# Performance work log

Measured on AMD Instinct MI355X. Metric: run time of the kernel, lower is better.

The kernel has to match this reference:

```python
import jax, jax.numpy as jnp
import numpy as np

E = 8        # n_experts
TOP_K = 2    # n_activated_experts
B, T, C = 4, 2048, 2048   # batch, seq, d_model
F = 5632     # expert FFN hidden (SwiGLU)


def setup_inputs() -> dict:
    key = jax.random.key(0)
    k = jax.random.split(key, 5)
    s = 0.02  # init scale keeps activations sane
    return {
        "x":  jax.random.normal(k[0], (B, T, C), jnp.float32),
        "Wg": jax.random.normal(k[1], (C, E), jnp.float32) * s,   # gate Linear (no bias)
        "W1": jax.random.normal(k[2], (E, C, F), jnp.float32) * s, # expert gate proj
        "W3": jax.random.normal(k[3], (E, C, F), jnp.float32) * s, # expert up proj
        "W2": jax.random.normal(k[4], (E, F, C), jnp.float32) * s, # expert down proj
    }


def _moe(x, Wg, W1, W3, W2, top_k=TOP_K, norm_probs=True):
    Bb, Tt, Cc = x.shape
    xf = x.reshape(-1, Cc)                                   # [N, C]
    logits = xf @ Wg                                         # [N, E]
    probs = jax.nn.softmax(logits.astype(jnp.float32), axis=-1)
    probs, indices = jax.lax.top_k(probs, top_k)             # [N, K]
    if norm_probs:
        probs = probs / probs.sum(axis=-1, keepdims=True)
    probs = probs.astype(x.dtype)
    N, Ee = xf.shape[0], W1.shape[0]
    # per-token combine weights: w[n, e] = prob if expert e selected for token n else 0
    # (top_k indices are distinct per token, so at most one add per (n, e))
    w = jnp.zeros((N, Ee), x.dtype).at[jnp.arange(N)[:, None], indices].add(probs)
    # scan over experts: weight-0 tokens contribute nothing, matching the sparse
    # masked dispatch/scatter-add of the original exactly.
    def body(y, ws):
        w1, w3, w2, we = ws                                   # we: [N]
        h = jax.nn.silu(xf @ w1) * (xf @ w3)                  # [N, F]
        return y + we[:, None] * (h @ w2), None
    y, _ = jax.lax.scan(body, jnp.zeros_like(xf), (W1, W3, W2, w.T))
    return y.reshape(Bb, Tt, Cc)


def reference(x, Wg, W1, W3, W2):
    return _moe(x, Wg, W1, W3, W2)
```

## Files before the change

kernel.cpp:

```cpp
#include <hip/hip_runtime.h>

#define N_TOK 8192
#define C_DIM 2048
#define F_DIM 5632
#define E_NUM 8
#define BK 64

#define BM 256
#define MAXT 72
#define BN1 128
#define GRID1 (MAXT * (F_DIM/BN1))
#define BN2 256
#define KSPLIT 2
#define GRID2 (MAXT * (C_DIM/BN2) * KSPLIT)
#define NT1 (C_DIM/BK)
#define NT2H (F_DIM/BK/KSPLIT)
#define KHALF (F_DIM/KSPLIT)

#define PRE_R 2048
#define PRE_T 45056
#define GRID_PRE (PRE_R + PRE_T)

typedef __attribute__((ext_vector_type(8))) short bf16x8;
typedef __attribute__((ext_vector_type(4))) float f32x4;

typedef const void __attribute__((address_space(1)))* gas1;
typedef void __attribute__((address_space(3)))* las3;

__device__ __forceinline__ unsigned short f2bf(float f){
  union { float f; unsigned u; } v; v.f = f;
  unsigned r = v.u + 0x7FFFu + ((v.u >> 16) & 1u);
  return (unsigned short)(r >> 16);
}

__device__ __forceinline__ void glds16(const unsigned short* g, unsigned short* l){
  __builtin_amdgcn_global_load_lds((gas1)g, (las3)l, 16, 0, 0);
}

#define MFMA_BF16 __builtin_amdgcn_mfma_f32_16x16x32_bf16

#define BAR1_VM(N) do{ asm volatile("s_waitcnt vmcnt(" #N ")" ::: "memory"); \
    __builtin_amdgcn_sched_barrier(0); __builtin_amdgcn_s_barrier(); \
    __builtin_amdgcn_sched_barrier(0); } while(0)
#define BAR2() do{ asm volatile("s_waitcnt lgkmcnt(0)" ::: "memory"); \
    __builtin_amdgcn_sched_barrier(0); __builtin_amdgcn_s_barrier(); \
    __builtin_amdgcn_sched_barrier(0); } while(0)

__global__ __launch_bounds__(256) void k_pre(
    const float* __restrict__ x, const float* __restrict__ Wg,
    const float* __restrict__ W1, const float* __restrict__ W3,
    int* __restrict__ cnt, int* __restrict__ list, float* __restrict__ p_slot,
    unsigned short* __restrict__ xb, unsigned short* __restrict__ wb13)
{
  __shared__ float t[64][65];
  int bid = blockIdx.x;
  int tid = threadIdx.x;

  if (bid < PRE_R){
    int wid = tid >> 6, lane = tid & 63;
    int n = bid * 4 + wid;
    int e = lane >> 3, sub = lane & 7;
    const float* xr = x + (size_t)n * C_DIM;
    float acc = 0.f;
    for (int i0 = sub*4; i0 < C_DIM; i0 += 32){
      float4 v = *(const float4*)&xr[i0];
      acc += v.x * Wg[(i0  )*E_NUM + e];
      acc += v.y * Wg[(i0+1)*E_NUM + e];
      acc += v.z * Wg[(i0+2)*E_NUM + e];
      acc += v.w * Wg[(i0+3)*E_NUM + e];
    }
    acc += __shfl_xor(acc, 1);
    acc += __shfl_xor(acc, 2);
    acc += __shfl_xor(acc, 4);
    float lg[E_NUM];
    #pragma unroll
    for (int j = 0; j < E_NUM; ++j) lg[j] = __shfl(acc, j*8);
    unsigned short* xbr = xb + (size_t)n * C_DIM;
    #pragma unroll
    for (int i0 = lane*4; i0 < C_DIM; i0 += 256){
      float4 v = *(const float4*)&xr[i0];
      ushort4 u; u.x = f2bf(v.x); u.y = f2bf(v.y); u.z = f2bf(v.z); u.w = f2bf(v.w);
      *(ushort4*)&xbr[i0] = u;
    }
    if (lane == 0){
      int e1 = 0; float m1 = lg[0];
      #pragma unroll
      for (int j = 1; j < E_NUM; ++j) if (lg[j] > m1){ m1 = lg[j]; e1 = j; }
      int e2 = -1; float m2 = -1e30f;
      #pragma unroll
      for (int j = 0; j < E_NUM; ++j) if (j != e1 && lg[j] > m2){ m2 = lg[j]; e2 = j; }
      float p1 = 1.f / (1.f + __expf(m2 - m1));
      float p2 = 1.f - p1;
      int pos1 = atomicAdd(&cnt[e1], 1);
      list[e1*N_TOK + pos1] = n*2;
      p_slot[n*2] = p1;
      int pos2 = atomicAdd(&cnt[e2], 1);
      list[e2*N_TOK + pos2] = n*2 + 1;
      p_slot[n*2 + 1] = p2;
    }
    return;
  }
  int rel = bid - PRE_R;
  int z = rel / 2816;
  int r2 = rel - z*2816;
  int fx = r2 % 88, cy = r2 / 88;
  const float* in = ((z < 8) ? W1 : W3) + (size_t)(z & 7) * C_DIM * F_DIM;
  unsigned short* out = wb13 + (size_t)z * C_DIM * F_DIM;
  int c0 = fx*64, r0 = cy*64;
  int tx = tid & 63, ty = tid >> 6;
  #pragma unroll
  for (int i = 0; i < 16; ++i){
    int r = ty + i*4;
    t[r][tx] = in[(size_t)(r0 + r) * F_DIM + c0 + tx];
  }
  __syncthreads();
  #pragma unroll
  for (int i = 0; i < 16; ++i){
    int cr = ty + i*4;
    out[(size_t)(c0 + cr) * C_DIM + r0 + tx] = f2bf(t[tx][cr]);
  }
}

__global__ void k_tw2(const float* __restrict__ W2, unsigned short* __restrict__ wb2){
  __shared__ float t[64][65];
  const float* in = W2 + (size_t)blockIdx.z * F_DIM * C_DIM;
  unsigned short* out = wb2 + (size_t)blockIdx.z * C_DIM * F_DIM;
  int c0 = blockIdx.x * 64, r0 = blockIdx.y * 64;
  int tx = threadIdx.x, ty = threadIdx.y;
  #pragma unroll
  for (int i = 0; i < 16; ++i){
    int r = ty + i*4;
    t[r][tx] = in[(size_t)(r0 + r) * C_DIM + c0 + tx];
  }
  __syncthreads();
  #pragma unroll
  for (int i = 0; i < 16; ++i){
    int cr = ty + i*4;
    out[(size_t)(c0 + cr) * F_DIM + r0 + tx] = f2bf(t[tx][cr]);
  }
}

__global__ void k_prefix(const int* __restrict__ cnt, int* __restrict__ meta){
  if (threadIdx.x == 0 && blockIdx.x == 0){
    int acc = 0, t = 0;
    for (int e = 0; e < E_NUM; ++e){
      meta[e] = acc; acc += cnt[e];
      int nt = (cnt[e] + BM - 1) / BM;
      for (int i = 0; i < nt; ++i) meta[16 + t++] = (e << 16) | i;
    }
    meta[8] = t;
  }
}

__global__ __launch_bounds__(512, 2) void k_gemm1(
    const unsigned short* __restrict__ xb,
    const unsigned short* __restrict__ wb1,
    const unsigned short* __restrict__ wb3,
    unsigned short* __restrict__ h,
    const int* __restrict__ cnt,
    const int* __restrict__ meta,
    const int* __restrict__ list)
{
  __shared__ __align__(16) unsigned short lds[2*32768];
  int o = blockIdx.x;
  int tid = threadIdx.x;

  int w = (o & 7) * (GRID1/8) + (o >> 3);
  int t = w % MAXT;
  int n0 = (w / MAXT) * BN1;
  if (t >= meta[8]) return;
  int info = meta[16 + t];
  int e  = info >> 16;
  int m0 = (info & 0xffff) * BM;
  int count = cnt[e];
  int hbase = meta[e];

  int lane = tid & 63, wid = tid >> 6;
  int wm = wid >> 1, wn = wid & 1;
  int l15 = lane & 15;
  int xc0 = (lane >> 4) ^ (lane & 7);
  int xc1 = xc0 ^ 4;

  int srow = tid >> 3;
  int swz = ((tid & 7) ^ (srow & 7)) * 8;
  const unsigned short* aP[4];
  #pragma unroll
  for (int u = 0; u < 4; ++u){
    int ts = list[e*N_TOK + m0 + u*64 + srow];
    int tok = (ts >> 1) & (N_TOK - 1);
    aP[u] = xb + (size_t)tok * C_DIM + swz;
  }
  const unsigned short* bP[4];
  #pragma unroll
  for (int u = 0; u < 4; ++u){
    const unsigned short* base = (u < 2) ? wb1 : wb3;
    bP[u] = base + ((size_t)e*F_DIM + n0 + (u & 1)*64 + srow) * C_DIM + swz;
  }
  int ldw = wid * 512;

  #define ST_A(u, kt) glds16(aP[u] + (kt)*BK, &lds[((kt)&1)*32768 + (u)*4096 + ldw])
  #define ST_B(u, kt) glds16(bP[u] + (kt)*BK, &lds[((kt)&1)*32768 + 16384 + (u)*4096 + ldw])
  #define READ_A(d, buf) do{ _Pragma("unroll") for (int m_ = 0; m_ < 4; ++m_){ \
      int row_ = wm*64 + m_*16 + l15; \
      d[m_][0] = *(const bf16x8*)&(buf)[row_*64 + xc0*8]; \
      d[m_][1] = *(const bf16x8*)&(buf)[row_*64 + xc1*8]; } }while(0)
  #define READ_B(d1, d3, buf, q) do{ int brow_ = wn*64 + (q)*16 + l15; \
      d1[0] = *(const bf16x8*)&(buf)[16384 + brow_*64 + xc0*8]; \
      d1[1] = *(const bf16x8*)&(buf)[16384 + brow_*64 + xc1*8]; \
      d3[0] = *(const bf16x8*)&(buf)[24576 + brow_*64 + xc0*8]; \
      d3[1] = *(const bf16x8*)&(buf)[24576 + brow_*64 + xc1*8]; }while(0)
  #define MFMA16(q, b1, b3) do{ _Pragma("unroll") for (int m_ = 0; m_ < 4; ++m_){ \
      acc1[m_][q] = MFMA_BF16(a[m_][0], b1[0], acc1[m_][q], 0, 0, 0); \
      acc1[m_][q] = MFMA_BF16(a[m_][1], b1[1], acc1[m_][q], 0, 0, 0); \
      acc3[m_][q] = MFMA_BF16(a[m_][0], b3[0], acc3[m_][q], 0, 0, 0); \
      acc3[m_][q] = MFMA_BF16(a[m_][1], b3[1], acc3[m_][q], 0, 0, 0); } }while(0)

  ST_A(0,0); ST_A(1,0); ST_A(2,0); ST_A(3,0);
  ST_B(0,0); ST_B(1,0); ST_B(2,0); ST_B(3,0);
  ST_A(0,1); ST_A(1,1); ST_A(2,1); ST_A(3,1);
  asm volatile("s_waitcnt vmcnt(4)" ::: "memory");
  __builtin_amdgcn_sched_barrier(0);
  __builtin_amdgcn_s_barrier();
  __builtin_amdgcn_sched_barrier(0);

  f32x4 zero = {0.f, 0.f, 0.f, 0.f};
  f32x4 acc1[4][4], acc3[4][4];
  #pragma unroll
  for (int m = 0; m < 4; ++m)
    #pragma unroll
    for (int q = 0; q < 4; ++q){ acc1[m][q] = zero; acc3[m][q] = zero; }

  bf16x8 a[4][2];
  READ_A(a, lds);
  bf16x8 bX1[2], bX3[2], bY1[2], bY3[2];
  READ_B(bX1, bX3, lds, 0);

  for (int kt = 0; kt < NT1; ++kt){
    const unsigned short* bufc = &lds[(kt & 1)*32768];
    const unsigned short* bufn = &lds[((kt+1) & 1)*32768];
    ST_B(0, kt+1); ST_B(1, kt+1); ST_B(2, kt+1); ST_B(3, kt+1);
    READ_B(bY1, bY3, bufc, 1);
    __builtin_amdgcn_s_setprio(1);
    MFMA16(0, bX1, bX3);
    __builtin_amdgcn_s_setprio(0);
    ST_A(0, kt+2); ST_A(1, kt+2);
    READ_B(bX1, bX3, bufc, 2);
    __builtin_amdgcn_s_setprio(1);
    MFMA16(1, bY1, bY3);
    __builtin_amdgcn_s_setprio(0);
    ST_A(2, kt+2); ST_A(3, kt+2);
    READ_B(bY1, bY3, bufc, 3);
    __builtin_amdgcn_s_setprio(1);
    MFMA16(2, bX1, bX3);
    __builtin_amdgcn_s_setprio(0);
    BAR1_VM(4);
    bf16x8 an[4][2];
    READ_A(an, bufn);
    READ_B(bX1, bX3, bufn, 0);
    __builtin_amdgcn_s_setprio(1);
    MFMA16(3, bY1, bY3);
    __builtin_amdgcn_s_setprio(0);
    BAR2();
    #pragma unroll
    for (int m = 0; m < 4; ++m){ a[m][0] = an[m][0]; a[m][1] = an[m][1]; }
  }
  asm volatile("s_waitcnt vmcnt(0)" ::: "memory");

  #pragma unroll
  for (int m = 0; m < 4; ++m){
    #pragma unroll
    for (int r = 0; r < 4; ++r){
      int rloc = m0 + wm*64 + m*16 + ((lane >> 4) * 4) + r;
      if (rloc < count){
        unsigned short* hrow = h + (size_t)(hbase + rloc) * F_DIM + n0 + wn*64 + l15;
        #pragma unroll
        for (int q = 0; q < 4; ++q){
          float v1 = acc1[m][q][r];
          float v3 = acc3[m][q][r];
          float hv = (v1 / (1.f + __expf(-v1))) * v3;
          hrow[q*16] = f2bf(hv);
        }
      }
    }
  }
  #undef ST_A
  #undef ST_B
  #undef READ_A
  #undef READ_B
  #undef MFMA16
}

__global__ __launch_bounds__(512, 2) void k_gemm2(
    const unsigned short* __restrict__ h,
    const unsigned short* __restrict__ wb2,
    unsigned short* __restrict__ ybuf,
    const int* __restrict__ cnt,
    const int* __restrict__ meta,
    const int* __restrict__ list)
{
  int o = blockIdx.x;
  int w = (o & 7) * (GRID2/8) + (o >> 3);
  int ks = w / (GRID2/KSPLIT);
  int r2 = w % (GRID2/KSPLIT);
  int t = r2 % MAXT;
  int n0 = (r2 / MAXT) * BN2;
  if (t >= meta[8]) return;
  int info = meta[16 + t];
  int e  = info >> 16;
  int m0 = (info & 0xffff) * BM;
  int count = cnt[e];
  int hbase = meta[e];

  __shared__ __align__(16) unsigned short lds[2*32768];

  int tid = threadIdx.x;
  int lane = tid & 63, wid = tid >> 6;
  int wm = wid >> 1, wn = wid & 1;
  int l15 = lane & 15;
  int xc0 = (lane >> 4) ^ (lane & 7);
  int xc1 = xc0 ^ 4;

  int srow = tid >> 3;
  int swz = ((tid & 7) ^ (srow & 7)) * 8;
  size_t kb0 = (size_t)ks * KHALF;
  const unsigned short* aP[4];
  #pragma unroll
  for (int u = 0; u < 4; ++u)
    aP[u] = h + (size_t)(hbase + m0 + u*64 + srow) * F_DIM + kb0 + swz;
  const unsigned short* bP[4];
  #pragma unroll
  for (int u = 0; u < 4; ++u)
    bP[u] = wb2 + ((size_t)e*C_DIM + n0 + u*64 + srow) * F_DIM + kb0 + swz;
  int ldw = wid * 512;

  #define ST_A2(u, kt) glds16(aP[u] + (kt)*BK, &lds[((kt)&1)*32768 + (u)*4096 + ldw])
  #define ST_B2(u, kt) glds16(bP[u] + (kt)*BK, &lds[((kt)&1)*32768 + 16384 + (u)*4096 + ldw])
  #define READ_A2(d, buf) do{ _Pragma("unroll") for (int m_ = 0; m_ < 4; ++m_){ \
      int row_ = wm*64 + m_*16 + l15; \
      d[m_][0] = *(const bf16x8*)&(buf)[row_*64 + xc0*8]; \
      d[m_][1] = *(const bf16x8*)&(buf)[row_*64 + xc1*8]; } }while(0)
  #define READ_B2(d, buf, q) do{ _Pragma("unroll") for (int j_ = 0; j_ < 2; ++j_){ \
      int brow_ = wn*128 + ((q)*2 + j_)*16 + l15; \
      d[j_][0] = *(const bf16x8*)&(buf)[16384 + brow_*64 + xc0*8]; \
      d[j_][1] = *(const bf16x8*)&(buf)[16384 + brow_*64 + xc1*8]; } }while(0)
  #define MFMA2(qb, d) do{ _Pragma("unroll") for (int m_ = 0; m_ < 4; ++m_) \
      _Pragma("unroll") for (int j_ = 0; j_ < 2; ++j_){ \
        acc[m_][(qb)*2+j_] = MFMA_BF16(a[m_][0], d[j_][0], acc[m_][(qb)*2+j_], 0, 0, 0); \
        acc[m_][(qb)*2+j_] = MFMA_BF16(a[m_][1], d[j_][1], acc[m_][(qb)*2+j_], 0, 0, 0); } }while(0)

  ST_A2(0,0); ST_A2(1,0); ST_A2(2,0); ST_A2(3,0);
  ST_B2(0,0); ST_B2(1,0); ST_B2(2,0); ST_B2(3,0);
  asm volatile("s_waitcnt vmcnt(4)" ::: "memory");
  ST_A2(0,1); ST_A2(1,1); ST_A2(2,1); ST_A2(3,1);
  ST_B2(0,1); ST_B2(2,1);
  asm volatile("s_waitcnt vmcnt(6)" ::: "memory");
  __builtin_amdgcn_sched_barrier(0);
  __builtin_amdgcn_s_barrier();
  __builtin_amdgcn_sched_barrier(0);

  f32x4 zero = {0.f, 0.f, 0.f, 0.f};
  f32x4 acc[4][8];
  #pragma unroll
  for (int m = 0; m < 4; ++m)
    #pragma unroll
    for (int nf = 0; nf < 8; ++nf) acc[m][nf] = zero;

  bf16x8 a[4][2];
  READ_A2(a, lds);
  bf16x8 bfX[2][2], bfY[2][2];
  READ_B2(bfX, lds, 0);

  for (int kt = 0; kt < NT2H; ++kt){
    const unsigned short* bufc = &lds[(kt & 1)*32768];
    const unsigned short* bufn = &lds[((kt+1) & 1)*32768];
    ST_B2(1, kt+1); ST_B2(3, kt+1);
    READ_B2(bfY, bufc, 1);
    __builtin_amdgcn_s_setprio(1);
    MFMA2(0, bfX);
    __builtin_amdgcn_s_setprio(0);
    ST_A2(0, kt+2); ST_A2(1, kt+2);
    READ_B2(bfX, bufc, 2);
    __builtin_amdgcn_s_setprio(1);
    MFMA2(1, bfY);
    __builtin_amdgcn_s_setprio(0);
    ST_A2(2, kt+2); ST_A2(3, kt+2);
    READ_B2(bfY, bufc, 3);
    __builtin_amdgcn_s_setprio(1);
    MFMA2(2, bfX);
    __builtin_amdgcn_s_setprio(0);
    ST_B2(0, kt+2); ST_B2(2, kt+2);
    BAR1_VM(6);
    bf16x8 an[4][2];
    READ_A2(an, bufn);
    READ_B2(bfX, bufn, 0);
    __builtin_amdgcn_s_setprio(1);
    MFMA2(3, bfY);
    __builtin_amdgcn_s_setprio(0);
    BAR2();
    #pragma unroll
    for (int m = 0; m < 4; ++m){ a[m][0] = an[m][0]; a[m][1] = an[m][1]; }
  }
  asm volatile("s_waitcnt vmcnt(0)" ::: "memory");

  #pragma unroll
  for (int m = 0; m < 4; ++m){
    #pragma unroll
    for (int r = 0; r < 4; ++r){
      int rloc = m0 + wm*64 + m*16 + ((lane >> 4) * 4) + r;
      if (rloc < count){
        int ts = list[e*N_TOK + rloc];
        unsigned short* yr = ybuf + ((size_t)ks*(2*N_TOK) + ts)*C_DIM + n0 + wn*128 + l15;
        #pragma unroll
        for (int nf = 0; nf < 8; ++nf)
          yr[nf*16] = f2bf(acc[m][nf][r]);
      }
    }
  }
  #undef ST_A2
  #undef ST_B2
  #undef READ_A2
  #undef READ_B2
  #undef MFMA2
}

__global__ __launch_bounds__(256) void k_combine(
    const unsigned short* __restrict__ ybuf,
    const float* __restrict__ p_slot,
    float* __restrict__ y)
{
  const int CW = C_DIM/8;
  int i = blockIdx.x * blockDim.x + threadIdx.x;
  int stride = gridDim.x * blockDim.x;
  const size_t KS_OFF = (size_t)(2*N_TOK) * C_DIM;
  for (; i < N_TOK*CW; i += stride){
    int n = i >> 8;
    int c0 = (i & 255) * 8;
    size_t b1 = (size_t)(2*n)   * C_DIM + c0;
    size_t b2 = (size_t)(2*n+1) * C_DIM + c0;
    ushort4 a0 = *(const ushort4*)&ybuf[b1];
    ushort4 a1 = *(const ushort4*)&ybuf[b1+4];
    ushort4 a2 = *(const ushort4*)&ybuf[KS_OFF + b1];
    ushort4 a3 = *(const ushort4*)&ybuf[KS_OFF + b1+4];
    ushort4 c2 = *(const ushort4*)&ybuf[b2];
    ushort4 c3 = *(const ushort4*)&ybuf[b2+4];
    ushort4 d2 = *(const ushort4*)&ybuf[KS_OFF + b2];
    ushort4 d3 = *(const ushort4*)&ybuf[KS_OFF + b2+4];
    float p1 = p_slot[2*n], p2 = p_slot[2*n+1];
    float out[8];
    #define B2F(u) __builtin_bit_cast(float, (unsigned)(u) << 16)
    out[0] = p1*(B2F(a0.x)+B2F(a2.x)) + p2*(B2F(c2.x)+B2F(d2.x));
    out[1] = p1*(B2F(a0.y)+B2F(a2.y)) + p2*(B2F(c2.y)+B2F(d2.y));
    out[2] = p1*(B2F(a0.z)+B2F(a2.z)) + p2*(B2F(c2.z)+B2F(d2.z));
    out[3] = p1*(B2F(a0.w)+B2F(a2.w)) + p2*(B2F(c2.w)+B2F(d2.w));
    out[4] = p1*(B2F(a1.x)+B2F(a3.x)) + p2*(B2F(c3.x)+B2F(d3.x));
    out[5] = p1*(B2F(a1.y)+B2F(a3.y)) + p2*(B2F(c3.y)+B2F(d3.y));
    out[6] = p1*(B2F(a1.z)+B2F(a3.z)) + p2*(B2F(c3.z)+B2F(d3.z));
    out[7] = p1*(B2F(a1.w)+B2F(a3.w)) + p2*(B2F(c3.w)+B2F(d3.w));
    #undef B2F
    float4* yo = (float4*)&y[(size_t)n * C_DIM + c0];
    yo[0] = *(float4*)&out[0];
    yo[1] = *(float4*)&out[4];
  }
}

extern "C" void kernel_launch(void* const* d_in, const int* in_sizes, int n_in,
                              void* d_out, int out_size, void* d_ws, size_t ws_size,
                              hipStream_t stream)
{
  const float* x  = (const float*)d_in[0];
  const float* Wg = (const float*)d_in[1];
  const float* W1 = (const float*)d_in[2];
  const float* W3 = (const float*)d_in[3];
  const float* W2 = (const float*)d_in[4];
  float* y = (float*)d_out;
  (void)in_sizes; (void)n_in; (void)out_size; (void)ws_size;

  char* ws = (char*)d_ws;
  size_t o = 0;
  auto alloc = [&](size_t bytes)->char* {
    char* p = ws + o;
    o = (o + bytes + 255) & ~(size_t)255;
    return p;
  };
  int*    cnt    = (int*)  alloc(E_NUM * 4);
  int*    meta   = (int*)  alloc(160 * 4);
  float*  p_slot = (float*)alloc((size_t)2*N_TOK * 4);
  int*    list   = (int*)  alloc((size_t)E_NUM*N_TOK * 4);
  unsigned short* xb  = (unsigned short*)alloc((size_t)N_TOK*C_DIM * 2 + 65536);
  unsigned short* wb1 = (unsigned short*)alloc((size_t)E_NUM*C_DIM*F_DIM * 2);
  unsigned short* wb3 = (unsigned short*)alloc((size_t)E_NUM*C_DIM*F_DIM * 2);
  unsigned short* wb2 = (unsigned short*)alloc((size_t)E_NUM*C_DIM*F_DIM * 2);
  unsigned short* h   = (unsigned short*)alloc((size_t)(2*N_TOK + 1024)*F_DIM * 2 + 65536);
  unsigned short* ybuf= (unsigned short*)alloc((size_t)KSPLIT*2*N_TOK*C_DIM * 2);
  (void)wb3;

  hipMemsetAsync(cnt, 0, E_NUM * 4, stream);
  k_pre<<<GRID_PRE, 256, 0, stream>>>(x, Wg, W1, W3, cnt, list, p_slot, xb, wb1);
  k_prefix<<<1, 64, 0, stream>>>(cnt, meta);
  k_tw2<<<dim3(C_DIM/64, F_DIM/64, E_NUM), dim3(64,4), 0, stream>>>(W2, wb2);
  k_gemm1<<<GRID1, 512, 0, stream>>>(xb, wb1, wb3, h, cnt, meta, list);
  k_gemm2<<<GRID2, 512, 0, stream>>>(h, wb2, ybuf, cnt, meta, list);
  k_combine<<<4096, 256, 0, stream>>>(ybuf, p_slot, y);
}
```

Baseline: 1.697 ms.

## Fold W2 transpose into pre kernel and remap GEMM tiles per XCD

The separate W2 transpose/bf16-convert kernel is merged into k_pre as extra blocks, which removes a launch and lets the W2 conversion share the grid with the W1/W3 conversion. The block-to-tile mapping in both GEMMs changes so that each XCD (blockIdx mod 8) gets a fixed set of M-tiles and sweeps all N-columns for them. This is meant to keep a tile's activation rows resident in one XCD's L2. It may also change how weight reuse and load balance fall across XCDs.

```diff
diff --git a/kernel.cpp b/kernel.cpp
--- a/kernel.cpp
+++ b/kernel.cpp
@@ -9,16 +9,18 @@
 #define BM 256
 #define MAXT 72
 #define BN1 128
-#define GRID1 (MAXT * (F_DIM/BN1))
+#define NN1 (F_DIM/BN1)
+#define GRID1 (MAXT * NN1)
 #define BN2 256
 #define KSPLIT 2
-#define GRID2 (MAXT * (C_DIM/BN2) * KSPLIT)
+#define NN2 (C_DIM/BN2)
+#define GRID2 (MAXT * NN2 * KSPLIT)
 #define NT1 (C_DIM/BK)
 #define NT2H (F_DIM/BK/KSPLIT)
 #define KHALF (F_DIM/KSPLIT)
 
 #define PRE_R 2048
-#define PRE_T 45056
+#define PRE_T 67584
 #define GRID_PRE (PRE_R + PRE_T)
 
 typedef __attribute__((ext_vector_type(8))) short bf16x8;
@@ -49,8 +51,10 @@
 __global__ __launch_bounds__(256) void k_pre(
     const float* __restrict__ x, const float* __restrict__ Wg,
     const float* __restrict__ W1, const float* __restrict__ W3,
+    const float* __restrict__ W2,
     int* __restrict__ cnt, int* __restrict__ list, float* __restrict__ p_slot,
-    unsigned short* __restrict__ xb, unsigned short* __restrict__ wb13)
+    unsigned short* __restrict__ xb, unsigned short* __restrict__ wb13,
+    unsigned short* __restrict__ wb2)
 {
   __shared__ float t[64][65];
   int bid = blockIdx.x;
@@ -103,40 +107,39 @@
   int rel = bid - PRE_R;
   int z = rel / 2816;
   int r2 = rel - z*2816;
-  int fx = r2 % 88, cy = r2 / 88;
-  const float* in = ((z < 8) ? W1 : W3) + (size_t)(z & 7) * C_DIM * F_DIM;
-  unsigned short* out = wb13 + (size_t)z * C_DIM * F_DIM;
-  int c0 = fx*64, r0 = cy*64;
   int tx = tid & 63, ty = tid >> 6;
-  #pragma unroll
-  for (int i = 0; i < 16; ++i){
-    int r = ty + i*4;
-    t[r][tx] = in[(size_t)(r0 + r) * F_DIM + c0 + tx];
-  }
-  __syncthreads();
-  #pragma unroll
-  for (int i = 0; i < 16; ++i){
-    int cr = ty + i*4;
-    out[(size_t)(c0 + cr) * C_DIM + r0 + tx] = f2bf(t[tx][cr]);
-  }
-}
-
-__global__ void k_tw2(const float* __restrict__ W2, unsigned short* __restrict__ wb2){
-  __shared__ float t[64][65];
-  const float* in = W2 + (size_t)blockIdx.z * F_DIM * C_DIM;
-  unsigned short* out = wb2 + (size_t)blockIdx.z * C_DIM * F_DIM;
-  int c0 = blockIdx.x * 64, r0 = blockIdx.y * 64;
-  int tx = threadIdx.x, ty = threadIdx.y;
-  #pragma unroll
-  for (int i = 0; i < 16; ++i){
-    int r = ty + i*4;
-    t[r][tx] = in[(size_t)(r0 + r) * C_DIM + c0 + tx];
-  }
-  __syncthreads();
-  #pragma unroll
-  for (int i = 0; i < 16; ++i){
-    int cr = ty + i*4;
-    out[(size_t)(c0 + cr) * F_DIM + r0 + tx] = f2bf(t[tx][cr]);
+  if (z < 16){
+    int fx = r2 % 88, cy = r2 / 88;
+    const float* in = ((z < 8) ? W1 : W3) + (size_t)(z & 7) * C_DIM * F_DIM;
+    unsigned short* out = wb13 + (size_t)z * C_DIM * F_DIM;
+    int c0 = fx*64, r0 = cy*64;
+    #pragma unroll
+    for (int i = 0; i < 16; ++i){
+      int r = ty + i*4;
+      t[r][tx] = in[(size_t)(r0 + r) * F_DIM + c0 + tx];
+    }
+    __syncthreads();
+    #pragma unroll
+    for (int i = 0; i < 16; ++i){
+      int cr = ty + i*4;
+      out[(size_t)(c0 + cr) * C_DIM + r0 + tx] = f2bf(t[tx][cr]);
+    }
+  } else {
+    int cx = r2 % 32, fy = r2 / 32;
+    const float* in = W2 + (size_t)(z - 16) * F_DIM * C_DIM;
+    unsigned short* out = wb2 + (size_t)(z - 16) * C_DIM * F_DIM;
+    int c0 = cx*64, r0 = fy*64;
+    #pragma unroll
+    for (int i = 0; i < 16; ++i){
+      int r = ty + i*4;
+      t[r][tx] = in[(size_t)(r0 + r) * C_DIM + c0 + tx];
+    }
+    __syncthreads();
+    #pragma unroll
+    for (int i = 0; i < 16; ++i){
+      int cr = ty + i*4;
+      out[(size_t)(c0 + cr) * F_DIM + r0 + tx] = f2bf(t[tx][cr]);
+    }
   }
 }
 
@@ -165,9 +168,9 @@
   int o = blockIdx.x;
   int tid = threadIdx.x;
 
-  int w = (o & 7) * (GRID1/8) + (o >> 3);
-  int t = w % MAXT;
-  int n0 = (w / MAXT) * BN1;
+  int xcd = o & 7, idx = o >> 3;
+  int t = (idx / NN1) * 8 + xcd;
+  int n0 = (idx % NN1) * BN1;
   if (t >= meta[8]) return;
   int info = meta[16 + t];
   int e  = info >> 16;
@@ -299,11 +302,12 @@
     const int* __restrict__ list)
 {
   int o = blockIdx.x;
-  int w = (o & 7) * (GRID2/8) + (o >> 3);
-  int ks = w / (GRID2/KSPLIT);
-  int r2 = w % (GRID2/KSPLIT);
-  int t = r2 % MAXT;
-  int n0 = (r2 / MAXT) * BN2;
+  int tid = threadIdx.x;
+  int xcd = o & 7, idx = o >> 3;
+  int ks = idx / 72;
+  int r2 = idx % 72;
+  int t = (r2 / NN2) * 8 + xcd;
+  int n0 = (r2 % NN2) * BN2;
   if (t >= meta[8]) return;
   int info = meta[16 + t];
   int e  = info >> 16;
@@ -313,7 +317,6 @@
 
   __shared__ __align__(16) unsigned short lds[2*32768];
 
-  int tid = threadIdx.x;
   int lane = tid & 63, wid = tid >> 6;
   int wm = wid >> 1, wn = wid & 1;
   int l15 = lane & 15;
@@ -495,9 +498,8 @@
   (void)wb3;
 
   hipMemsetAsync(cnt, 0, E_NUM * 4, stream);
-  k_pre<<<GRID_PRE, 256, 0, stream>>>(x, Wg, W1, W3, cnt, list, p_slot, xb, wb1);
+  k_pre<<<GRID_PRE, 256, 0, stream>>>(x, Wg, W1, W3, W2, cnt, list, p_slot, xb, wb1, wb2);
   k_prefix<<<1, 64, 0, stream>>>(cnt, meta);
-  k_tw2<<<dim3(C_DIM/64, F_DIM/64, E_NUM), dim3(64,4), 0, stream>>>(W2, wb2);
   k_gemm1<<<GRID1, 512, 0, stream>>>(xb, wb1, wb3, h, cnt, meta, list);
   k_gemm2<<<GRID2, 512, 0, stream>>>(h, wb2, ybuf, cnt, meta, list);
   k_combine<<<4096, 256, 0, stream>>>(ybuf, p_slot, y);
```

Result: no change. 1.731 ms (+2.0%).
